# Kernel tuning notes

Measured on AMD Instinct MI355X. Metric: run time of the kernel, lower is better.

The kernel has to match this reference:

```python
import jax, jax.numpy as jnp
import numpy as np

N = 8192
IN_F = 512
OUT_F = 64
NEG_INF = -9e15

def setup_inputs() -> dict:
    key = jax.random.key(0)
    k1, k2, k3, k4 = jax.random.split(key, 4)
    node_features = jax.random.normal(k1, (N, IN_F), dtype=jnp.float32)
    adjacency_matrix = jax.random.randint(k2, (N, N), 0, 2, dtype=jnp.int32)
    # Xavier-uniform-like init (gain 1.414), scale irrelevant for correctness
    w_bound = 1.414 * np.sqrt(6.0 / (IN_F + OUT_F))
    a_bound = 1.414 * np.sqrt(6.0 / (2 * OUT_F + 1))
    weight_matrix = jax.random.uniform(k3, (IN_F, OUT_F), minval=-w_bound, maxval=w_bound, dtype=jnp.float32)
    attention_vector = jax.random.uniform(k4, (2 * OUT_F, 1), minval=-a_bound, maxval=a_bound, dtype=jnp.float32)
    return {
        "node_features": node_features,
        "adjacency_matrix": adjacency_matrix,
        "weight_matrix": weight_matrix,
        "attention_vector": attention_vector,
    }

def reference(node_features, adjacency_matrix, weight_matrix, attention_vector):
    # h: [N, F] transformed features
    h = node_features @ weight_matrix
    # score[i, j] = h[i] . a_left + h[j] . a_right
    a_left = attention_vector[:OUT_F, 0]   # [F]
    a_right = attention_vector[OUT_F:, 0]  # [F]
    scores = (h @ a_left)[:, None] + (h @ a_right)[None, :]  # [N, N]
    # NOTE: source defines leaky_relu but never applies it in forward — faithful omission.
    masked = jnp.where(adjacency_matrix > 0, scores, NEG_INF)
    attn = jax.nn.softmax(masked, axis=1)  # [N, N]
    # dropout p=0 / inference: no-op
    out = attn @ h  # [N, F]
    return jax.nn.elu(out)  # concat=True path
```

## Files before the change

kernel.cpp:

```cpp
#include <hip/hip_runtime.h>
#include <hip/hip_bf16.h>
#include <cstdint>

#define NN      8192
#define OF      64
#define KC      16
#define CW      512
#define SLROWS  65
#define SLSTR   520
#define PSTR    65

#define OFF_HW  0
#define OFF_P   1310720

typedef __attribute__((ext_vector_type(8))) short  s16x8;
typedef __attribute__((ext_vector_type(4))) float  f32x4;

__device__ __forceinline__ unsigned short f2bf(float f) {
  unsigned int u = __float_as_uint(f);
  unsigned int r = (u + 0x7FFFu + ((u >> 16) & 1u)) >> 16;
  return (unsigned short)r;
}

__global__ __launch_bounds__(256) void k1_hw(const float* __restrict__ X,
                                             const float* __restrict__ W,
                                             const float* __restrict__ att,
                                             unsigned short* __restrict__ HW) {
  __shared__ float xs[16 * 516];
  __shared__ float ws[64 * 68];
  int t = threadIdx.x;
  int rb = blockIdx.x * 16;

  {
    const float4* src = (const float4*)(X + (size_t)rb * 512);
#pragma unroll
    for (int s = 0; s < 8; ++s) {
      int lid = s * 256 + t;
      int row = lid >> 7, kseg = lid & 127;
      *(float4*)&xs[row * 516 + kseg * 4] = src[row * 128 + kseg];
    }
  }

  int row = t >> 4, tx = t & 15;
  float4 acc = {0.f, 0.f, 0.f, 0.f};
  for (int kc = 0; kc < 8; ++kc) {
    __syncthreads();
#pragma unroll
    for (int s = 0; s < 4; ++s) {
      int lid = s * 256 + t;
      int k = lid >> 4, cs = lid & 15;
      *(float4*)&ws[k * 68 + cs * 4] =
          *(const float4*)(W + (size_t)(kc * 64 + k) * 64 + cs * 4);
    }
    __syncthreads();
#pragma unroll 16
    for (int k = 0; k < 64; ++k) {
      float x = xs[row * 516 + kc * 64 + k];
      float4 w4 = *(const float4*)&ws[k * 68 + tx * 4];
      acc.x += x * w4.x; acc.y += x * w4.y;
      acc.z += x * w4.z; acc.w += x * w4.w;
    }
  }

  float v = acc.x * att[64 + tx * 4]     + acc.y * att[64 + tx * 4 + 1] +
            acc.z * att[64 + tx * 4 + 2] + acc.w * att[64 + tx * 4 + 3];
#pragma unroll
  for (int m = 8; m > 0; m >>= 1) v += __shfl_xor(v, m, 64);
  float e = expf(v);

  int j = rb + row;
  unsigned short* hw = HW + j;
  float hv[4] = {acc.x, acc.y, acc.z, acc.w};
#pragma unroll
  for (int c = 0; c < 4; ++c)
    hw[(size_t)(tx * 4 + c) * NN] = f2bf(e * hv[c]);
  if (tx == 0) hw[(size_t)64 * NN] = f2bf(e);
}

__device__ __forceinline__ s16x8 cvt8(int4 a, int4 b) {
  union { unsigned u[4]; s16x8 v; } rr;
  rr.u[0] = (unsigned)(a.x | (a.y << 16)) * 0x3F80u;
  rr.u[1] = (unsigned)(a.z | (a.w << 16)) * 0x3F80u;
  rr.u[2] = (unsigned)(b.x | (b.y << 16)) * 0x3F80u;
  rr.u[3] = (unsigned)(b.z | (b.w << 16)) * 0x3F80u;
  return rr.v;
}

__global__ __launch_bounds__(256, 2) void k3_gat(const int* __restrict__ A,
                                                 const unsigned short* __restrict__ HW,
                                                 float* __restrict__ P) {
  __shared__ unsigned short bt[SLROWS * SLSTR];

  int t = threadIdx.x;
  int kc = blockIdx.x & 15;
  int mg = blockIdx.x >> 4;
  int lane = t & 63, w = t >> 6;
  int l15 = lane & 15, q = lane >> 4;
  int k0 = kc * CW;

#pragma unroll
  for (int i = 0; i < 16; ++i) {
    int lid = i * 256 + t;
    int row = lid >> 6, sg = lid & 63;
    *(uint4*)&bt[row * SLSTR + sg * 8] =
        *(const uint4*)(HW + (size_t)row * NN + k0 + sg * 8);
  }
  if (t < 64)
    *(uint4*)&bt[64 * SLSTR + t * 8] =
        *(const uint4*)(HW + (size_t)64 * NN + k0 + t * 8);
  __syncthreads();

  float* Pp = P + (size_t)kc * NN * PSTR;
  const s16x8 zero8 = {0, 0, 0, 0, 0, 0, 0, 0};

  for (int mt = 0; mt < 4; ++mt) {
    int rowM = mg * 256 + w * 64 + mt * 16;
    const int* ar = A + (size_t)(rowM + l15) * NN + k0 + q * 8;

    f32x4 acc[5];
#pragma unroll
    for (int tt = 0; tt < 5; ++tt) acc[tt] = 0.f;

    int4 c0 = *(const int4*)(ar);
    int4 c1 = *(const int4*)(ar + 4);
    int4 c2 = *(const int4*)(ar + 32);
    int4 c3 = *(const int4*)(ar + 36);
    ar += 64;

#pragma unroll
    for (int step = 0; step < 8; ++step) {
      int4 n0, n1, n2, n3;
      if (step != 7) {
        n0 = *(const int4*)(ar);
        n1 = *(const int4*)(ar + 4);
        n2 = *(const int4*)(ar + 32);
        n3 = *(const int4*)(ar + 36);
        ar += 64;
      }

      s16x8 af0 = cvt8(c0, c1);
      s16x8 af1 = cvt8(c2, c3);

#pragma unroll
      for (int ks = 0; ks < 2; ++ks) {
        s16x8 af = ks ? af1 : af0;
        int kb = step * 64 + ks * 32 + q * 8;
#pragma unroll
        for (int tt = 0; tt < 4; ++tt) {
          s16x8 b = *(const s16x8*)&bt[(tt * 16 + l15) * SLSTR + kb];
          acc[tt] = __builtin_amdgcn_mfma_f32_16x16x32_bf16(af, b, acc[tt], 0, 0, 0);
        }
        s16x8 b4 = *(const s16x8*)&bt[64 * SLSTR + kb];
        b4 = (l15 == 0) ? b4 : zero8;
        acc[4] = __builtin_amdgcn_mfma_f32_16x16x32_bf16(af, b4, acc[4], 0, 0, 0);
      }

      c0 = n0; c1 = n1; c2 = n2; c3 = n3;
    }

    int rb = rowM + q * 4;
#pragma unroll
    for (int tt = 0; tt < 4; ++tt)
#pragma unroll
      for (int rg = 0; rg < 4; ++rg)
        Pp[(size_t)(rb + rg) * PSTR + tt * 16 + l15] = acc[tt][rg];
    if (l15 == 0)
#pragma unroll
      for (int rg = 0; rg < 4; ++rg)
        Pp[(size_t)(rb + rg) * PSTR + 64] = acc[4][rg];
  }
}

__global__ __launch_bounds__(256) void k4_fin(const float* __restrict__ P,
                                              float* __restrict__ out) {
  int g = blockIdx.x * 256 + threadIdx.x;
  int i = g >> 6, c = g & 63;
  float num = 0.f, S = 0.f;
#pragma unroll
  for (int kc = 0; kc < KC; ++kc) {
    const float* p = P + (size_t)kc * NN * PSTR + (size_t)i * PSTR;
    num += p[c];
    S   += p[64];
  }
  float x = num / S;
  out[g] = x > 0.f ? x : expm1f(x);
}

extern "C" void kernel_launch(void* const* d_in, const int* in_sizes, int n_in,
                              void* d_out, int out_size, void* d_ws, size_t ws_size,
                              hipStream_t stream) {
  const float* X  = (const float*)d_in[0];
  const int*   A  = (const int*)d_in[1];
  const float* W  = (const float*)d_in[2];
  const float* av = (const float*)d_in[3];
  float* out = (float*)d_out;

  char* ws = (char*)d_ws;
  unsigned short* HW = (unsigned short*)(ws + OFF_HW);
  float*          P  = (float*)(ws + OFF_P);

  k1_hw<<<NN / 16, 256, 0, stream>>>(X, W, av, HW);
  k3_gat<<<512, 256, 0, stream>>>(A, HW, P);
  k4_fin<<<(size_t)NN * OF / 256, 256, 0, stream>>>(P, out);
}
```

Baseline: 451.7 us.

## Restructure GAT aggregation with coalesced adjacency loads staged through LDS

The aggregation kernel now launches four times as many blocks, each covering 64 rows instead of 256. Adjacency rows are loaded with contiguous per-row int4 reads, triple-buffered in registers, converted to bf16 and transposed through a small LDS tile before the MFMA. The HW slice in LDS uses an XOR swizzle instead of padding to avoid bank conflicts. This is meant to fix poorly coalesced strided adjacency reads and raise parallelism, at the cost of reloading the HW slice per block and adding two barriers per step.

New measurement: 396.3 us. 12.3% less time.

```diff
diff --git a/kernel.cpp b/kernel.cpp
--- a/kernel.cpp
+++ b/kernel.cpp
@@ -6,8 +6,7 @@
 #define OF      64
 #define KC      16
 #define CW      512
-#define SLROWS  65
-#define SLSTR   520
+#define ASTR    72
 #define PSTR    65
 
 #define OFF_HW  0
@@ -20,6 +19,11 @@
   unsigned int u = __float_as_uint(f);
   unsigned int r = (u + 0x7FFFu + ((u >> 16) & 1u)) >> 16;
   return (unsigned short)r;
+}
+
+__device__ __forceinline__ void lds_barrier() {
+  __builtin_amdgcn_s_waitcnt(0xC07F);
+  __builtin_amdgcn_s_barrier();
 }
 
 __global__ __launch_bounds__(256) void k1_hw(const float* __restrict__ X,
@@ -77,19 +81,11 @@
   if (tx == 0) hw[(size_t)64 * NN] = f2bf(e);
 }
 
-__device__ __forceinline__ s16x8 cvt8(int4 a, int4 b) {
-  union { unsigned u[4]; s16x8 v; } rr;
-  rr.u[0] = (unsigned)(a.x | (a.y << 16)) * 0x3F80u;
-  rr.u[1] = (unsigned)(a.z | (a.w << 16)) * 0x3F80u;
-  rr.u[2] = (unsigned)(b.x | (b.y << 16)) * 0x3F80u;
-  rr.u[3] = (unsigned)(b.z | (b.w << 16)) * 0x3F80u;
-  return rr.v;
-}
-
 __global__ __launch_bounds__(256, 2) void k3_gat(const int* __restrict__ A,
                                                  const unsigned short* __restrict__ HW,
                                                  float* __restrict__ P) {
-  __shared__ unsigned short bt[SLROWS * SLSTR];
+  __shared__ unsigned short bt[65 * 512];
+  __shared__ unsigned short at[64 * ASTR];
 
   int t = threadIdx.x;
   int kc = blockIdx.x & 15;
@@ -97,78 +93,93 @@
   int lane = t & 63, w = t >> 6;
   int l15 = lane & 15, q = lane >> 4;
   int k0 = kc * CW;
-
-#pragma unroll
-  for (int i = 0; i < 16; ++i) {
-    int lid = i * 256 + t;
-    int row = lid >> 6, sg = lid & 63;
-    *(uint4*)&bt[row * SLSTR + sg * 8] =
-        *(const uint4*)(HW + (size_t)row * NN + k0 + sg * 8);
-  }
-  if (t < 64)
-    *(uint4*)&bt[64 * SLSTR + t * 8] =
-        *(const uint4*)(HW + (size_t)64 * NN + k0 + t * 8);
-  __syncthreads();
+  int rowM = mg * 64;
+
+  const int* ap[4];
+#pragma unroll
+  for (int i = 0; i < 4; ++i)
+    ap[i] = A + (size_t)(rowM + w * 16 + i * 4 + q) * NN + k0 + l15 * 4;
+
+  int4 av[3][4];
+#pragma unroll
+  for (int i = 0; i < 4; ++i) av[0][i] = *(const int4*)(ap[i]);
+#pragma unroll
+  for (int i = 0; i < 4; ++i) av[1][i] = *(const int4*)(ap[i] + 64);
+
+#pragma unroll
+  for (int rds = 0; rds < 16; ++rds) {
+    int lid = rds * 256 + t;
+    int row = lid >> 6, ch = lid & 63;
+    uint4 v = *(const uint4*)(HW + (size_t)row * NN + k0 + ch * 8);
+    *(uint4*)&bt[row * 512 + ((ch ^ (row & 7)) * 8)] = v;
+  }
+  if (t < 64) {
+    uint4 v = *(const uint4*)(HW + (size_t)64 * NN + k0 + t * 8);
+    *(uint4*)&bt[64 * 512 + t * 8] = v;
+  }
+
+  int swz = l15 & 7;
+  int bb[4][2];
+#pragma unroll
+  for (int tt = 0; tt < 4; ++tt)
+#pragma unroll
+    for (int ks = 0; ks < 2; ++ks)
+      bb[tt][ks] = ((tt * 16 + l15) * 512 + (((ks * 4 + q) ^ swz) * 8)) * 2;
+  int eb0 = (64 * 512 + q * 8) * 2;
+  int eb1 = (64 * 512 + (4 + q) * 8) * 2;
+  int ab  = ((w * 16 + l15) * ASTR + q * 8) * 2;
+
+  f32x4 acc[5];
+#pragma unroll
+  for (int tt = 0; tt < 5; ++tt) acc[tt] = 0.f;
+  const s16x8 zero8 = {0, 0, 0, 0, 0, 0, 0, 0};
+
+#pragma unroll
+  for (int s = 0; s < 8; ++s) {
+    lds_barrier();
+#pragma unroll
+    for (int i = 0; i < 4; ++i) {
+      int4 vv = av[s % 3][i];
+      uint2 p;
+      p.x = (unsigned)(vv.x | (vv.y << 16)) * 0x3F80u;
+      p.y = (unsigned)(vv.z | (vv.w << 16)) * 0x3F80u;
+      *(uint2*)((char*)at + (((w * 16 + i * 4 + q) * ASTR + l15 * 4) * 2)) = p;
+    }
+    if (s < 6) {
+#pragma unroll
+      for (int i = 0; i < 4; ++i)
+        av[(s + 2) % 3][i] = *(const int4*)(ap[i] + (s + 2) * 64);
+    }
+    lds_barrier();
+
+    s16x8 af0 = *(const s16x8*)((char*)at + ab);
+    s16x8 af1 = *(const s16x8*)((char*)at + ab + 64);
+    int so = s * 128;
+#pragma unroll
+    for (int ks = 0; ks < 2; ++ks) {
+      s16x8 af = ks ? af1 : af0;
+#pragma unroll
+      for (int tt = 0; tt < 4; ++tt) {
+        s16x8 b = *(const s16x8*)((char*)bt + bb[tt][ks] + so);
+        acc[tt] = __builtin_amdgcn_mfma_f32_16x16x32_bf16(af, b, acc[tt], 0, 0, 0);
+      }
+      s16x8 b4 = *(const s16x8*)((char*)bt + (ks ? eb1 : eb0) + so);
+      b4 = (l15 == 0) ? b4 : zero8;
+      acc[4] = __builtin_amdgcn_mfma_f32_16x16x32_bf16(af, b4, acc[4], 0, 0, 0);
+    }
+  }
 
   float* Pp = P + (size_t)kc * NN * PSTR;
-  const s16x8 zero8 = {0, 0, 0, 0, 0, 0, 0, 0};
-
-  for (int mt = 0; mt < 4; ++mt) {
-    int rowM = mg * 256 + w * 64 + mt * 16;
-    const int* ar = A + (size_t)(rowM + l15) * NN + k0 + q * 8;
-
-    f32x4 acc[5];
-#pragma unroll
-    for (int tt = 0; tt < 5; ++tt) acc[tt] = 0.f;
-
-    int4 c0 = *(const int4*)(ar);
-    int4 c1 = *(const int4*)(ar + 4);
-    int4 c2 = *(const int4*)(ar + 32);
-    int4 c3 = *(const int4*)(ar + 36);
-    ar += 64;
-
-#pragma unroll
-    for (int step = 0; step < 8; ++step) {
-      int4 n0, n1, n2, n3;
-      if (step != 7) {
-        n0 = *(const int4*)(ar);
-        n1 = *(const int4*)(ar + 4);
-        n2 = *(const int4*)(ar + 32);
-        n3 = *(const int4*)(ar + 36);
-        ar += 64;
-      }
-
-      s16x8 af0 = cvt8(c0, c1);
-      s16x8 af1 = cvt8(c2, c3);
-
-#pragma unroll
-      for (int ks = 0; ks < 2; ++ks) {
-        s16x8 af = ks ? af1 : af0;
-        int kb = step * 64 + ks * 32 + q * 8;
-#pragma unroll
-        for (int tt = 0; tt < 4; ++tt) {
-          s16x8 b = *(const s16x8*)&bt[(tt * 16 + l15) * SLSTR + kb];
-          acc[tt] = __builtin_amdgcn_mfma_f32_16x16x32_bf16(af, b, acc[tt], 0, 0, 0);
-        }
-        s16x8 b4 = *(const s16x8*)&bt[64 * SLSTR + kb];
-        b4 = (l15 == 0) ? b4 : zero8;
-        acc[4] = __builtin_amdgcn_mfma_f32_16x16x32_bf16(af, b4, acc[4], 0, 0, 0);
-      }
-
-      c0 = n0; c1 = n1; c2 = n2; c3 = n3;
-    }
-
-    int rb = rowM + q * 4;
-#pragma unroll
-    for (int tt = 0; tt < 4; ++tt)
-#pragma unroll
-      for (int rg = 0; rg < 4; ++rg)
-        Pp[(size_t)(rb + rg) * PSTR + tt * 16 + l15] = acc[tt][rg];
-    if (l15 == 0)
-#pragma unroll
-      for (int rg = 0; rg < 4; ++rg)
-        Pp[(size_t)(rb + rg) * PSTR + 64] = acc[4][rg];
-  }
+  int rb = rowM + w * 16 + q * 4;
+#pragma unroll
+  for (int tt = 0; tt < 4; ++tt)
+#pragma unroll
+    for (int rg = 0; rg < 4; ++rg)
+      Pp[(size_t)(rb + rg) * PSTR + tt * 16 + l15] = acc[tt][rg];
+  if (l15 == 0)
+#pragma unroll
+    for (int rg = 0; rg < 4; ++rg)
+      Pp[(size_t)(rb + rg) * PSTR + 64] = acc[4][rg];
 }
 
 __global__ __launch_bounds__(256) void k4_fin(const float* __restrict__ P,
@@ -200,6 +211,6 @@
   float*          P  = (float*)(ws + OFF_P);
 
   k1_hw<<<NN / 16, 256, 0, stream>>>(X, W, av, HW);
-  k3_gat<<<512, 256, 0, stream>>>(A, HW, P);
+  k3_gat<<<128 * KC, 256, 0, stream>>>(A, HW, P);
   k4_fin<<<(size_t)NN * OF / 256, 256, 0, stream>>>(P, out);
 }
```
